# Optimization experiments

Measured on AMD Instinct MI355X. Metric: run time of the kernel, lower is better.

Reference implementation:

```python
import jax, jax.numpy as jnp
import numpy as np

B, Hh, Ww, C = 16, 56, 56, 256
NH, WS, SS = 8, 7, 3
HD = C // NH
N = WS * WS
SCALE = HD ** -0.5
EPS = 1e-5


def _rel_pos_index():
    coords = np.stack(np.meshgrid(np.arange(WS), np.arange(WS), indexing='ij'))  # (2, ws, ws)
    cf = coords.reshape(2, -1)
    rc = (cf[:, :, None] - cf[:, None, :]).transpose(1, 2, 0).astype(np.int64)  # (N, N, 2)
    rc[:, :, 0] += WS - 1
    rc[:, :, 1] += WS - 1
    rc[:, :, 0] *= 2 * WS - 1
    return jnp.asarray(rc.sum(-1))  # (N, N)

REL_IDX = _rel_pos_index()


def _shift_mask():
    # standard Swin SW-MSA mask for cyclic shift
    img = np.zeros((1, Hh, Ww, 1), dtype=np.float32)
    cnt = 0
    for hs in (slice(0, -WS), slice(-WS, -SS), slice(-SS, None)):
        for ws_ in (slice(0, -WS), slice(-WS, -SS), slice(-SS, None)):
            img[:, hs, ws_, :] = cnt
            cnt += 1
    mw = img.reshape(1, Hh // WS, WS, Ww // WS, WS, 1).transpose(0, 1, 3, 2, 4, 5).reshape(-1, N)
    am = mw[:, None, :] - mw[:, :, None]
    return jnp.asarray(np.where(am != 0, -100.0, 0.0).astype(np.float32))  # (nW, N, N)


def _ln(x, g, b):
    mu = x.mean(-1, keepdims=True)
    var = ((x - mu) ** 2).mean(-1, keepdims=True)
    return (x - mu) * jax.lax.rsqrt(var + EPS) * g + b


def setup_inputs() -> dict:
    key = jax.random.key(0)
    ks = jax.random.split(key, 8)
    return {
        'x': jax.random.normal(ks[0], (B, Hh * Ww, C), jnp.float32),
        'mask': _shift_mask(),
        'norm1_g': jnp.ones((C,), jnp.float32),
        'norm1_b': jnp.zeros((C,), jnp.float32),
        'qkv_w': jax.random.normal(ks[1], (3 * C, C), jnp.float32) * 0.02,
        'qkv_b': jnp.zeros((3 * C,), jnp.float32),
        'rel_bias': jax.random.normal(ks[2], ((2 * WS - 1) ** 2, NH), jnp.float32) * 0.02,
        'proj_w': jax.random.normal(ks[3], (C, C), jnp.float32) * 0.02,
        'proj_b': jnp.zeros((C,), jnp.float32),
        'norm2_g': jnp.ones((C,), jnp.float32),
        'norm2_b': jnp.zeros((C,), jnp.float32),
        'fc1_w': jax.random.normal(ks[4], (4 * C, C), jnp.float32) * 0.02,
        'fc1_b': jnp.zeros((4 * C,), jnp.float32),
        'fc2_w': jax.random.normal(ks[5], (C, 4 * C), jnp.float32) * 0.02,
        'fc2_b': jnp.zeros((C,), jnp.float32),
    }


def reference(x, mask, norm1_g, norm1_b, qkv_w, qkv_b, rel_bias, proj_w, proj_b,
              norm2_g, norm2_b, fc1_w, fc1_b, fc2_w, fc2_b):
    shortcut = x
    h = _ln(x, norm1_g, norm1_b).reshape(B, Hh, Ww, C)
    # cyclic shift
    h = jnp.roll(h, (-SS, -SS), axis=(1, 2))
    # window partition -> (B*nW, N, C)
    hw = h.reshape(B, Hh // WS, WS, Ww // WS, WS, C).transpose(0, 1, 3, 2, 4, 5).reshape(-1, N, C)
    # qkv projection
    qkv = (hw @ qkv_w.T + qkv_b).reshape(-1, N, 3, NH, HD).transpose(2, 0, 3, 1, 4)
    q, k, v = qkv[0] * SCALE, qkv[1], qkv[2]  # (Bw, NH, N, HD)
    attn = jnp.einsum('bhnd,bhmd->bhnm', q, k)  # (Bw, NH, N, N)
    rpb = rel_bias[REL_IDX.reshape(-1)].reshape(N, N, NH).transpose(2, 0, 1)
    attn = attn + rpb[None]
    nW = mask.shape[0]
    attn = attn.reshape(B, nW, NH, N, N) + mask[None, :, None]
    attn = jax.nn.softmax(attn.reshape(-1, NH, N, N), axis=-1)
    o = jnp.einsum('bhnm,bhmd->bhnd', attn, v).transpose(0, 2, 1, 3).reshape(-1, N, C)
    o = o @ proj_w.T + proj_b
    # window reverse
    o = o.reshape(B, Hh // WS, Ww // WS, WS, WS, C).transpose(0, 1, 3, 2, 4, 5).reshape(B, Hh, Ww, C)
    o = jnp.roll(o, (SS, SS), axis=(1, 2)).reshape(B, Hh * Ww, C)
    x = shortcut + o
    h2 = _ln(x, norm2_g, norm2_b)
    h2 = jax.nn.gelu(h2 @ fc1_w.T + fc1_b, approximate=False)
    return x + (h2 @ fc2_w.T + fc2_b)
```

## Files before the change

### kernel.cpp

```cpp
#include <hip/hip_runtime.h>
#include <cmath>

#define B_    16
#define HH    56
#define WWI   56
#define C_    256
#define NH_   8
#define WS_   7
#define SS_   3
#define HD_   32
#define NTOK  50176
#define NN    49
#define SCALE_ 0.17677669529663689f
#define EPS_  1e-5f

typedef __bf16  bf16x8  __attribute__((ext_vector_type(8)));
typedef float   f32x4   __attribute__((ext_vector_type(4)));
typedef unsigned short ushort8v __attribute__((ext_vector_type(8)));

__device__ __forceinline__ unsigned short f2bf(float f) {
    unsigned int u = __float_as_uint(f);
    unsigned int r = u + 0x7FFFu + ((u >> 16) & 1u);
    return (unsigned short)(r >> 16);
}
__device__ __forceinline__ float bf2f(unsigned short h) {
    return __uint_as_float(((unsigned int)h) << 16);
}
__device__ __forceinline__ float gelu_t(float x) {
    float t = 0.7978845608028654f * (x + 0.044715f * x * x * x);
    float e = __expf(2.0f * t);
    float th = 1.0f - 2.0f * __builtin_amdgcn_rcpf(e + 1.0f);
    return 0.5f * x * (1.0f + th);
}

__device__ __forceinline__ void gload_lds16(const unsigned short* g, unsigned short* l) {
    __builtin_amdgcn_global_load_lds(
        (const __attribute__((address_space(1))) unsigned int*)g,
        (__attribute__((address_space(3))) unsigned int*)l, 16, 0, 0);
}

__global__ __launch_bounds__(256) void convw_k(
    const float* __restrict__ qkvw, const float* __restrict__ projw,
    const float* __restrict__ fc1w, const float* __restrict__ fc2w,
    unsigned short* __restrict__ dst)
{
    int i = blockIdx.x * 256 + threadIdx.x;
    float v;
    if      (i < 196608) v = qkvw[i];
    else if (i < 262144) v = projw[i - 196608];
    else if (i < 524288) v = fc1w[i - 262144];
    else                 v = fc2w[i - 524288];
    dst[i] = f2bf(v);
}

__global__ __launch_bounds__(256) void cb_k(
    const float* __restrict__ mask, const float* __restrict__ relb,
    unsigned short* __restrict__ cb)
{
    int s = blockIdx.x;
    int wi = s >> 3, head = s & 7;
    for (int p = threadIdx.x; p < 2408; p += 256) {
        float v = 0.0f;
        if (p < 2401) {
            int i = p / NN, j = p - i * NN;
            int di = i / 7 - j / 7 + 6, dj = i % 7 - j % 7 + 6;
            v = relb[(di * 13 + dj) * NH_ + head] + mask[(size_t)wi * 2401 + p];
        }
        cb[(size_t)s * 2408 + p] = f2bf(v);
    }
}

__global__ __launch_bounds__(256) void ln_k(
    const float* __restrict__ x, const float* __restrict__ g,
    const float* __restrict__ bta, unsigned short* __restrict__ dst, int shifted)
{
    int wave = threadIdx.x >> 6, lane = threadIdx.x & 63;
    int tok = blockIdx.x * 4 + wave;
    const float4 v = *(const float4*)(x + (size_t)tok * C_ + lane * 4);
    float s = v.x + v.y + v.z + v.w;
    float q = v.x*v.x + v.y*v.y + v.z*v.z + v.w*v.w;
    for (int o = 32; o > 0; o >>= 1) { s += __shfl_xor(s, o, 64); q += __shfl_xor(q, o, 64); }
    float mu  = s * (1.0f / C_);
    float var = q * (1.0f / C_) - mu * mu;
    float rs  = rsqrtf(var + EPS_);
    float4 gg = *(const float4*)(g   + lane * 4);
    float4 bb = *(const float4*)(bta + lane * 4);
    float y0 = (v.x - mu) * rs * gg.x + bb.x;
    float y1 = (v.y - mu) * rs * gg.y + bb.y;
    float y2 = (v.z - mu) * rs * gg.z + bb.z;
    float y3 = (v.w - mu) * rs * gg.w + bb.w;
    size_t di;
    if (shifted) {
        int b = tok / 3136, p = tok % 3136;
        int ph = p / 56, pw = p % 56;
        int sh = ph - SS_; if (sh < 0) sh += HH;
        int sw = pw - SS_; if (sw < 0) sw += WWI;
        int bw = b * 64 + (sh / WS_) * 8 + (sw / WS_);
        int n  = (sh % WS_) * WS_ + (sw % WS_);
        di = ((size_t)bw * NN + n) * C_ + lane * 4;
    } else {
        di = (size_t)tok * C_ + lane * 4;
    }
    unsigned int lo = (unsigned int)f2bf(y0) | ((unsigned int)f2bf(y1) << 16);
    unsigned int hi = (unsigned int)f2bf(y2) | ((unsigned int)f2bf(y3) << 16);
    uint2 u; u.x = lo; u.y = hi;
    *(uint2*)(dst + di) = u;
}

template<int EPI, int NT>
__global__ __launch_bounds__(256) void gemm_k(
    const unsigned short* __restrict__ A, const unsigned short* __restrict__ Bt,
    int K, const float* __restrict__ bias,
    const float* __restrict__ resid, float* __restrict__ outF,
    unsigned short* __restrict__ outQ, unsigned short* __restrict__ outK,
    unsigned short* __restrict__ outV)
{
    __shared__ __align__(16) unsigned char smem[49152];
    const int tid = threadIdx.x;
    const int lin = blockIdx.x;
    const int xcd = lin & 7, t = lin >> 3;
    const int m0 = (xcd * 49 + t / NT) * 128;
    const int n0 = (t % NT) * 128;
    const int wave = tid >> 6, lane = tid & 63, quad = lane >> 4, l16 = lane & 15;
    const int wm = wave >> 1, wn = wave & 1;
    const int r0 = tid >> 2;
    const int c0 = (((tid & 3) ^ ((tid >> 3) & 3)) * 8);

    const size_t gA0 = (size_t)(m0 + r0) * K + c0;
    const size_t gA1 = (size_t)(m0 + r0 + 64) * K + c0;
    const size_t gB0 = (size_t)(n0 + r0) * K + c0;
    const size_t gB1 = (size_t)(n0 + r0 + 64) * K + c0;
    const int woff = wave * 512;
    const int sw8 = (quad ^ ((l16 >> 1) & 3)) * 8;

    f32x4 acc[4][4] = {};
    const int nk = K >> 5;
    #pragma unroll
    for (int p = 0; p < 2; ++p) {
        unsigned short* sA = (unsigned short*)(smem + p * 16384);
        unsigned short* sB = sA + 4096;
        const int kp = p << 5;
        gload_lds16(A + gA0 + kp, sA + woff);
        gload_lds16(A + gA1 + kp, sA + woff + 2048);
        gload_lds16(Bt + gB0 + kp, sB + woff);
        gload_lds16(Bt + gB1 + kp, sB + woff + 2048);
    }
    int bufc = 0;
    for (int kk = 0; kk < nk; ++kk) {
        if (kk + 2 < nk) {
            int bufn = bufc + 2; if (bufn >= 3) bufn -= 3;
            unsigned short* sA = (unsigned short*)(smem + bufn * 16384);
            unsigned short* sB = sA + 4096;
            const int k2 = (kk + 2) << 5;
            gload_lds16(A + gA0 + k2, sA + woff);
            gload_lds16(A + gA1 + k2, sA + woff + 2048);
            gload_lds16(Bt + gB0 + k2, sB + woff);
            gload_lds16(Bt + gB1 + k2, sB + woff + 2048);
            __asm volatile("s_waitcnt vmcnt(8)\n\ts_barrier" ::: "memory");
        } else if (kk + 1 < nk) {
            __asm volatile("s_waitcnt vmcnt(4)\n\ts_barrier" ::: "memory");
        } else {
            __asm volatile("s_waitcnt vmcnt(0)\n\ts_barrier" ::: "memory");
        }
        const unsigned short* sA = (const unsigned short*)(smem + bufc * 16384);
        const unsigned short* sB = sA + 4096;
        bf16x8 af[4], bfr[4];
        #pragma unroll
        for (int tt = 0; tt < 4; ++tt) {
            af[tt]  = __builtin_bit_cast(bf16x8, *(const ushort8v*)(sA + (wm * 64 + tt * 16 + l16) * 32 + sw8));
            bfr[tt] = __builtin_bit_cast(bf16x8, *(const ushort8v*)(sB + (wn * 64 + tt * 16 + l16) * 32 + sw8));
        }
        #pragma unroll
        for (int mt = 0; mt < 4; ++mt)
            #pragma unroll
            for (int nt = 0; nt < 4; ++nt)
                acc[mt][nt] = __builtin_amdgcn_mfma_f32_16x16x32_bf16(af[mt], bfr[nt], acc[mt][nt], 0, 0, 0);
        __asm volatile("s_barrier" ::: "memory");
        if (++bufc == 3) bufc = 0;
    }

    float b4[4];
    #pragma unroll
    for (int nt = 0; nt < 4; ++nt) b4[nt] = bias[n0 + wn * 64 + nt * 16 + l16];

    if (EPI == 0 || EPI == 2) {
        unsigned short (*swB)[136] = (unsigned short (*)[136])smem;
        const int seg = n0 >> 8;
        const float qs = (EPI == 0 && seg == 0) ? SCALE_ : 1.0f;
        #pragma unroll
        for (int mt = 0; mt < 4; ++mt)
            #pragma unroll
            for (int nt = 0; nt < 4; ++nt)
                #pragma unroll
                for (int r = 0; r < 4; ++r) {
                    float v = acc[mt][nt][r] + b4[nt];
                    if (EPI == 0) v *= qs; else v = gelu_t(v);
                    swB[wm * 64 + mt * 16 + quad * 4 + r][wn * 64 + nt * 16 + l16] = f2bf(v);
                }
        __syncthreads();
        if (EPI == 0) {
            unsigned short* dstp = seg == 0 ? outQ : (seg == 1 ? outK : outV);
            const int nbase = n0 & 255;
            for (int tt = tid; tt < 2048; tt += 256) {
                int row = tt >> 4, c8 = (tt & 15) * 8;
                int m = m0 + row, bw = m / NN, nw = m - bw * NN;
                int cc = nbase + c8;
                uint4 u = *(uint4*)&swB[row][c8];
                *(uint4*)&dstp[(((size_t)bw * NH_ + (cc >> 5)) * NN + nw) * HD_ + (cc & 31)] = u;
            }
        } else {
            for (int tt = tid; tt < 2048; tt += 256) {
                int row = tt >> 4, c8 = (tt & 15) * 8;
                uint4 u = *(uint4*)&swB[row][c8];
                *(uint4*)&outQ[(size_t)(m0 + row) * 1024 + n0 + c8] = u;
            }
        }
    } else {
        float (*swF)[132] = (float (*)[132])smem;
        #pragma unroll
        for (int p = 0; p < 2; ++p) {
            __syncthreads();
            if (wm == p) {
                #pragma unroll
                for (int mt = 0; mt < 4; ++mt)
                    #pragma unroll
                    for (int nt = 0; nt < 4; ++nt)
                        #pragma unroll
                        for (int r = 0; r < 4; ++r)
                            swF[mt * 16 + quad * 4 + r][wn * 64 + nt * 16 + l16] = acc[mt][nt][r] + b4[nt];
            }
            __syncthreads();
            for (int tt = tid; tt < 2048; tt += 256) {
                int rl = tt >> 5, c4 = (tt & 31) * 4;
                size_t adr;
                if (EPI == 1) {
                    int m = m0 + p * 64 + rl, bw = m / NN, nw = m - bw * NN;
                    int b = bw >> 6, wi = bw & 63;
                    int sh = (wi >> 3) * WS_ + nw / WS_;
                    int sw = (wi & 7) * WS_ + nw % WS_;
                    int ph = sh + SS_; if (ph >= HH)  ph -= HH;
                    int pw = sw + SS_; if (pw >= WWI) pw -= WWI;
                    adr = ((size_t)b * 3136 + ph * 56 + pw) * C_ + n0 + c4;
                } else {
                    adr = (size_t)(m0 + p * 64 + rl) * C_ + n0 + c4;
                }
                float4 u = *(float4*)&swF[rl][c4];
                const float4 rr = (EPI == 1) ? *(const float4*)&resid[adr]
                                             : *(const float4*)&outF[adr];
                u.x += rr.x; u.y += rr.y; u.z += rr.z; u.w += rr.w;
                *(float4*)&outF[adr] = u;
            }
        }
    }
}

__global__ __launch_bounds__(256) void attn_k(
    const unsigned short* __restrict__ qb, const unsigned short* __restrict__ kb,
    const unsigned short* __restrict__ vb, const unsigned short* __restrict__ cb,
    unsigned short* __restrict__ ob)
{
    __shared__ unsigned short qs[64][40];
    __shared__ unsigned short ks[64][40];
    __shared__ unsigned short vt[32][72];
    __shared__ unsigned short sp[64][72];
    __shared__ unsigned short cbs[2408];
    const int tid = threadIdx.x;
    const int bw = blockIdx.x >> 3, head = blockIdx.x & 7;
    const size_t base = (size_t)blockIdx.x * (NN * HD_);

    for (int t = tid; t < 588; t += 256) {
        int seg = t / 196, idx = t - seg * 196;
        int e = idx * 8;
        const unsigned short* src = (seg == 0 ? qb : seg == 1 ? kb : vb) + base + e;
        uint4 u = *(const uint4*)src;
        if (seg == 0)      *(uint4*)&qs[e >> 5][e & 31] = u;
        else if (seg == 1) *(uint4*)&ks[e >> 5][e & 31] = u;
        else {
            int n = e >> 5, hd = e & 31;
            const unsigned short* pu = (const unsigned short*)&u;
            #pragma unroll
            for (int uu = 0; uu < 8; ++uu) vt[hd + uu][n] = pu[uu];
        }
    }
    {
        const unsigned short* cbase = cb + (size_t)(((bw & 63) * 8 + head)) * 2408;
        for (int t = tid; t < 301; t += 256)
            *(uint4*)&cbs[t * 8] = *(const uint4*)(cbase + t * 8);
        for (int t = tid; t < 480; t += 256) vt[t / 15][NN + t % 15] = 0;
    }
    __syncthreads();

    const int wave = tid >> 6, lane = tid & 63, quad = lane >> 4, l16 = lane & 15;
    const f32x4 zz = {};

    bf16x8 afq = __builtin_bit_cast(bf16x8, *(const ushort8v*)&qs[wave * 16 + l16][quad * 8]);
    f32x4 s4[4];
    #pragma unroll
    for (int jt = 0; jt < 4; ++jt) {
        bf16x8 bk = __builtin_bit_cast(bf16x8, *(const ushort8v*)&ks[jt * 16 + l16][quad * 8]);
        s4[jt] = __builtin_amdgcn_mfma_f32_16x16x32_bf16(afq, bk, zz, 0, 0, 0);
    }

    #pragma unroll
    for (int r = 0; r < 4; ++r) {
        int i = wave * 16 + quad * 4 + r;
        float vals[4];
        #pragma unroll
        for (int jt = 0; jt < 4; ++jt) {
            int j = jt * 16 + l16;
            vals[jt] = (i < NN && j < NN) ? s4[jt][r] + bf2f(cbs[i * NN + j]) : -1e30f;
        }
        float mx = fmaxf(fmaxf(vals[0], vals[1]), fmaxf(vals[2], vals[3]));
        #pragma unroll
        for (int o = 1; o < 16; o <<= 1) mx = fmaxf(mx, __shfl_xor(mx, o, 64));
        float e[4], sum = 0.0f;
        #pragma unroll
        for (int jt = 0; jt < 4; ++jt) { e[jt] = __expf(vals[jt] - mx); sum += e[jt]; }
        #pragma unroll
        for (int o = 1; o < 16; o <<= 1) sum += __shfl_xor(sum, o, 64);
        float inv = 1.0f / sum;
        #pragma unroll
        for (int jt = 0; jt < 4; ++jt) sp[i][jt * 16 + l16] = f2bf(e[jt] * inv);
    }
    __syncthreads();

    bf16x8 ap[2];
    #pragma unroll
    for (int kt = 0; kt < 2; ++kt)
        ap[kt] = __builtin_bit_cast(bf16x8, *(const ushort8v*)&sp[wave * 16 + l16][kt * 32 + quad * 8]);
    f32x4 o4[2] = {};
    #pragma unroll
    for (int nt = 0; nt < 2; ++nt)
        #pragma unroll
        for (int kt = 0; kt < 2; ++kt) {
            bf16x8 bv = __builtin_bit_cast(bf16x8, *(const ushort8v*)&vt[nt * 16 + l16][kt * 32 + quad * 8]);
            o4[nt] = __builtin_amdgcn_mfma_f32_16x16x32_bf16(ap[kt], bv, o4[nt], 0, 0, 0);
        }
    #pragma unroll
    for (int nt = 0; nt < 2; ++nt)
        #pragma unroll
        for (int r = 0; r < 4; ++r) {
            int i = wave * 16 + quad * 4 + r;
            if (i < NN)
                ob[((size_t)bw * NN + i) * C_ + head * HD_ + nt * 16 + l16] = f2bf(o4[nt][r]);
        }
}

extern "C" void kernel_launch(void* const* d_in, const int* in_sizes, int n_in,
                              void* d_out, int out_size, void* d_ws, size_t ws_size,
                              hipStream_t stream)
{
    const float* x     = (const float*)d_in[0];
    const float* mask  = (const float*)d_in[1];
    const float* n1g   = (const float*)d_in[2];
    const float* n1b   = (const float*)d_in[3];
    const float* qkvw  = (const float*)d_in[4];
    const float* qkvb  = (const float*)d_in[5];
    const float* relb  = (const float*)d_in[6];
    const float* projw = (const float*)d_in[7];
    const float* projb = (const float*)d_in[8];
    const float* n2g   = (const float*)d_in[9];
    const float* n2b   = (const float*)d_in[10];
    const float* fc1w  = (const float*)d_in[11];
    const float* fc1b  = (const float*)d_in[12];
    const float* fc2w  = (const float*)d_in[13];
    const float* fc2b  = (const float*)d_in[14];
    float* out = (float*)d_out;

    unsigned short* wq = (unsigned short*)d_ws;
    unsigned short* wp = wq + 196608;
    unsigned short* w1 = wq + 262144;
    unsigned short* w2 = wq + 524288;
    unsigned short* hw = wq + 786432;
    unsigned short* qb = hw + 12845056;
    unsigned short* kb = qb + 12845056;
    unsigned short* vb = kb + 12845056;
    unsigned short* ob = vb + 12845056;
    unsigned short* h2 = ob + 12845056;
    unsigned short* a1 = h2 + 12845056;
    unsigned short* cbt = a1;

    convw_k<<<3072, 256, 0, stream>>>(qkvw, projw, fc1w, fc2w, wq);
    cb_k<<<512, 256, 0, stream>>>(mask, relb, cbt);
    ln_k<<<12544, 256, 0, stream>>>(x, n1g, n1b, hw, 1);
    gemm_k<0, 6><<<392 * 6, 256, 0, stream>>>(hw, wq, 256, qkvb, nullptr, nullptr, qb, kb, vb);
    attn_k<<<8192, 256, 0, stream>>>(qb, kb, vb, cbt, ob);
    gemm_k<1, 2><<<392 * 2, 256, 0, stream>>>(ob, wp, 256, projb, x, out, nullptr, nullptr, nullptr);
    ln_k<<<12544, 256, 0, stream>>>(out, n2g, n2b, h2, 0);
    gemm_k<2, 8><<<392 * 8, 256, 0, stream>>>(h2, w1, 256, fc1b, nullptr, nullptr, a1, nullptr, nullptr);
    gemm_k<3, 2><<<392 * 2, 256, 0, stream>>>(a1, w2, 1024, fc2b, nullptr, out, nullptr, nullptr, nullptr);
}
```

Measured before the change: 375.2 us.

## Replace direct-to-LDS triple buffering with register-staged double-buffered GEMM pipeline

```diff
diff --git a/kernel.cpp b/kernel.cpp
--- a/kernel.cpp
+++ b/kernel.cpp
@@ -31,12 +31,6 @@
     float e = __expf(2.0f * t);
     float th = 1.0f - 2.0f * __builtin_amdgcn_rcpf(e + 1.0f);
     return 0.5f * x * (1.0f + th);
-}
-
-__device__ __forceinline__ void gload_lds16(const unsigned short* g, unsigned short* l) {
-    __builtin_amdgcn_global_load_lds(
-        (const __attribute__((address_space(1))) unsigned int*)g,
-        (__attribute__((address_space(3))) unsigned int*)l, 16, 0, 0);
 }
 
 __global__ __launch_bounds__(256) void convw_k(
@@ -115,7 +109,7 @@
     unsigned short* __restrict__ outQ, unsigned short* __restrict__ outK,
     unsigned short* __restrict__ outV)
 {
-    __shared__ __align__(16) unsigned char smem[49152];
+    __shared__ __align__(16) unsigned char smem[34816];
     const int tid = threadIdx.x;
     const int lin = blockIdx.x;
     const int xcd = lin & 7, t = lin >> 3;
@@ -126,58 +120,70 @@
     const int r0 = tid >> 2;
     const int c0 = (((tid & 3) ^ ((tid >> 3) & 3)) * 8);
 
-    const size_t gA0 = (size_t)(m0 + r0) * K + c0;
-    const size_t gA1 = (size_t)(m0 + r0 + 64) * K + c0;
-    const size_t gB0 = (size_t)(n0 + r0) * K + c0;
-    const size_t gB1 = (size_t)(n0 + r0 + 64) * K + c0;
-    const int woff = wave * 512;
+    const unsigned short* pA0 = A  + (size_t)(m0 + r0) * K + c0;
+    const unsigned short* pA1 = A  + (size_t)(m0 + r0 + 64) * K + c0;
+    const unsigned short* pB0 = Bt + (size_t)(n0 + r0) * K + c0;
+    const unsigned short* pB1 = Bt + (size_t)(n0 + r0 + 64) * K + c0;
+    unsigned char* stg = smem + tid * 16;
     const int sw8 = (quad ^ ((l16 >> 1) & 3)) * 8;
 
     f32x4 acc[4][4] = {};
     const int nk = K >> 5;
-    #pragma unroll
-    for (int p = 0; p < 2; ++p) {
-        unsigned short* sA = (unsigned short*)(smem + p * 16384);
-        unsigned short* sB = sA + 4096;
-        const int kp = p << 5;
-        gload_lds16(A + gA0 + kp, sA + woff);
-        gload_lds16(A + gA1 + kp, sA + woff + 2048);
-        gload_lds16(Bt + gB0 + kp, sB + woff);
-        gload_lds16(Bt + gB1 + kp, sB + woff + 2048);
-    }
-    int bufc = 0;
-    for (int kk = 0; kk < nk; ++kk) {
+
+    uint4 rA0[2], rA1[2], rB0[2], rB1[2];
+    rA0[0] = *(const uint4*)(pA0);      rA1[0] = *(const uint4*)(pA1);
+    rB0[0] = *(const uint4*)(pB0);      rB1[0] = *(const uint4*)(pB1);
+    rA0[1] = *(const uint4*)(pA0 + 32); rA1[1] = *(const uint4*)(pA1 + 32);
+    rB0[1] = *(const uint4*)(pB0 + 32); rB1[1] = *(const uint4*)(pB1 + 32);
+    *(uint4*)(stg        ) = rA0[0];
+    *(uint4*)(stg +  4096) = rA1[0];
+    *(uint4*)(stg +  8192) = rB0[0];
+    *(uint4*)(stg + 12288) = rB1[0];
+    __asm volatile("s_waitcnt lgkmcnt(0)\n\ts_barrier" ::: "memory");
+
+    #define COMPUTE(p_) { \
+        const unsigned short* sA = (const unsigned short*)(smem + (p_) * 16384); \
+        const unsigned short* sB = sA + 4096; \
+        bf16x8 af[4], bfr[4]; \
+        _Pragma("unroll") \
+        for (int tt = 0; tt < 4; ++tt) { \
+            af[tt]  = __builtin_bit_cast(bf16x8, *(const ushort8v*)(sA + (wm * 64 + tt * 16 + l16) * 32 + sw8)); \
+            bfr[tt] = __builtin_bit_cast(bf16x8, *(const ushort8v*)(sB + (wn * 64 + tt * 16 + l16) * 32 + sw8)); \
+        } \
+        _Pragma("unroll") \
+        for (int mt = 0; mt < 4; ++mt) \
+            _Pragma("unroll") \
+            for (int nt = 0; nt < 4; ++nt) \
+                acc[mt][nt] = __builtin_amdgcn_mfma_f32_16x16x32_bf16(af[mt], bfr[nt], acc[mt][nt], 0, 0, 0); }
+
+    for (int kk = 0; kk < nk; kk += 2) {
         if (kk + 2 < nk) {
-            int bufn = bufc + 2; if (bufn >= 3) bufn -= 3;
-            unsigned short* sA = (unsigned short*)(smem + bufn * 16384);
-            unsigned short* sB = sA + 4096;
             const int k2 = (kk + 2) << 5;
-            gload_lds16(A + gA0 + k2, sA + woff);
-            gload_lds16(A + gA1 + k2, sA + woff + 2048);
-            gload_lds16(Bt + gB0 + k2, sB + woff);
-            gload_lds16(Bt + gB1 + k2, sB + woff + 2048);
-            __asm volatile("s_waitcnt vmcnt(8)\n\ts_barrier" ::: "memory");
-        } else if (kk + 1 < nk) {
-            __asm volatile("s_waitcnt vmcnt(4)\n\ts_barrier" ::: "memory");
-        } else {
-            __asm volatile("s_waitcnt vmcnt(0)\n\ts_barrier" ::: "memory");
-        }
-        const unsigned short* sA = (const unsigned short*)(smem + bufc * 16384);
-        const unsigned short* sB = sA + 4096;
-        bf16x8 af[4], bfr[4];
-        #pragma unroll
-        for (int tt = 0; tt < 4; ++tt) {
-            af[tt]  = __builtin_bit_cast(bf16x8, *(const ushort8v*)(sA + (wm * 64 + tt * 16 + l16) * 32 + sw8));
-            bfr[tt] = __builtin_bit_cast(bf16x8, *(const ushort8v*)(sB + (wn * 64 + tt * 16 + l16) * 32 + sw8));
-        }
-        #pragma unroll
-        for (int mt = 0; mt < 4; ++mt)
-            #pragma unroll
-            for (int nt = 0; nt < 4; ++nt)
-                acc[mt][nt] = __builtin_amdgcn_mfma_f32_16x16x32_bf16(af[mt], bfr[nt], acc[mt][nt], 0, 0, 0);
-        __asm volatile("s_barrier" ::: "memory");
-        if (++bufc == 3) bufc = 0;
-    }
+            rA0[0] = *(const uint4*)(pA0 + k2); rA1[0] = *(const uint4*)(pA1 + k2);
+            rB0[0] = *(const uint4*)(pB0 + k2); rB1[0] = *(const uint4*)(pB1 + k2);
+        }
+        COMPUTE(0);
+        *(uint4*)(stg + 16384        ) = rA0[1];
+        *(uint4*)(stg + 16384 +  4096) = rA1[1];
+        *(uint4*)(stg + 16384 +  8192) = rB0[1];
+        *(uint4*)(stg + 16384 + 12288) = rB1[1];
+        __asm volatile("s_waitcnt lgkmcnt(0)\n\ts_barrier" ::: "memory");
+
+        if (kk + 3 < nk) {
+            const int k3 = (kk + 3) << 5;
+            rA0[1] = *(const uint4*)(pA0 + k3); rA1[1] = *(const uint4*)(pA1 + k3);
+            rB0[1] = *(const uint4*)(pB0 + k3); rB1[1] = *(const uint4*)(pB1 + k3);
+        }
+        COMPUTE(1);
+        if (kk + 2 < nk) {
+            *(uint4*)(stg        ) = rA0[0];
+            *(uint4*)(stg +  4096) = rA1[0];
+            *(uint4*)(stg +  8192) = rB0[0];
+            *(uint4*)(stg + 12288) = rB1[0];
+        }
+        __asm volatile("s_waitcnt lgkmcnt(0)\n\ts_barrier" ::: "memory");
+    }
+    #undef COMPUTE
 
     float b4[4];
     #pragma unroll
```

Measured after the change: 691.9 us. +84.4%, slower.

## Enlarge GEMM tiles to 256x128 and remap workgroups across XCDs

Applied to the files above, without the earlier changes.

```diff
diff --git a/kernel.cpp b/kernel.cpp
--- a/kernel.cpp
+++ b/kernel.cpp
@@ -108,76 +108,75 @@
 }
 
 template<int EPI, int NT>
-__global__ __launch_bounds__(256) void gemm_k(
+__global__ __launch_bounds__(256, 2) void gemm_k(
     const unsigned short* __restrict__ A, const unsigned short* __restrict__ Bt,
     int K, const float* __restrict__ bias,
     const float* __restrict__ resid, float* __restrict__ outF,
     unsigned short* __restrict__ outQ, unsigned short* __restrict__ outK,
     unsigned short* __restrict__ outV)
 {
-    __shared__ __align__(16) unsigned char smem[49152];
+    __shared__ __align__(16) unsigned char smem[73728];
     const int tid = threadIdx.x;
-    const int lin = blockIdx.x;
-    const int xcd = lin & 7, t = lin >> 3;
-    const int m0 = (xcd * 49 + t / NT) * 128;
-    const int n0 = (t % NT) * 128;
+    const int nwg = 196 * NT;
+    const int xcd = blockIdx.x & 7, t = blockIdx.x >> 3;
+    const int wg = xcd * (nwg >> 3) + t;
+    const int m0 = (wg / NT) * 256;
+    const int n0 = (wg % NT) * 128;
     const int wave = tid >> 6, lane = tid & 63, quad = lane >> 4, l16 = lane & 15;
     const int wm = wave >> 1, wn = wave & 1;
-    const int r0 = tid >> 2;
-    const int c0 = (((tid & 3) ^ ((tid >> 3) & 3)) * 8);
-
-    const size_t gA0 = (size_t)(m0 + r0) * K + c0;
-    const size_t gA1 = (size_t)(m0 + r0 + 64) * K + c0;
-    const size_t gB0 = (size_t)(n0 + r0) * K + c0;
-    const size_t gB1 = (size_t)(n0 + r0 + 64) * K + c0;
-    const int woff = wave * 512;
+    const int c0 = (((lane & 3) ^ ((lane >> 3) & 3)) * 8);
+    const unsigned short* p6[6];
+    unsigned dof[6];
+    #pragma unroll
+    for (int i = 0; i < 6; ++i) {
+        int id = wave * 6 + i;
+        p6[i] = (id < 16 ? A  + (size_t)(m0 + id * 16 + (lane >> 2)) * K
+                         : Bt + (size_t)(n0 + (id - 16) * 16 + (lane >> 2)) * K) + c0;
+        dof[i] = id * 1024;
+    }
     const int sw8 = (quad ^ ((l16 >> 1) & 3)) * 8;
 
-    f32x4 acc[4][4] = {};
+    f32x4 acc[8][4] = {};
     const int nk = K >> 5;
-    #pragma unroll
-    for (int p = 0; p < 2; ++p) {
-        unsigned short* sA = (unsigned short*)(smem + p * 16384);
-        unsigned short* sB = sA + 4096;
-        const int kp = p << 5;
-        gload_lds16(A + gA0 + kp, sA + woff);
-        gload_lds16(A + gA1 + kp, sA + woff + 2048);
-        gload_lds16(Bt + gB0 + kp, sB + woff);
-        gload_lds16(Bt + gB1 + kp, sB + woff + 2048);
-    }
+
+    #define STAGE(kt_, p_) { \
+        unsigned char* bb_ = smem + (p_) * 24576; \
+        const int ko_ = (kt_) << 5; \
+        _Pragma("unroll") \
+        for (int i_ = 0; i_ < 6; ++i_) \
+            gload_lds16(p6[i_] + ko_, (unsigned short*)(bb_ + dof[i_])); }
+
+    STAGE(0, 0);
+    STAGE(1, 1);
     int bufc = 0;
     for (int kk = 0; kk < nk; ++kk) {
         if (kk + 2 < nk) {
             int bufn = bufc + 2; if (bufn >= 3) bufn -= 3;
-            unsigned short* sA = (unsigned short*)(smem + bufn * 16384);
-            unsigned short* sB = sA + 4096;
-            const int k2 = (kk + 2) << 5;
-            gload_lds16(A + gA0 + k2, sA + woff);
-            gload_lds16(A + gA1 + k2, sA + woff + 2048);
-            gload_lds16(Bt + gB0 + k2, sB + woff);
-            gload_lds16(Bt + gB1 + k2, sB + woff + 2048);
-            __asm volatile("s_waitcnt vmcnt(8)\n\ts_barrier" ::: "memory");
+            STAGE(kk + 2, bufn);
+            __asm volatile("s_waitcnt vmcnt(12)\n\ts_barrier" ::: "memory");
         } else if (kk + 1 < nk) {
-            __asm volatile("s_waitcnt vmcnt(4)\n\ts_barrier" ::: "memory");
+            __asm volatile("s_waitcnt vmcnt(6)\n\ts_barrier" ::: "memory");
         } else {
             __asm volatile("s_waitcnt vmcnt(0)\n\ts_barrier" ::: "memory");
         }
-        const unsigned short* sA = (const unsigned short*)(smem + bufc * 16384);
-        const unsigned short* sB = sA + 4096;
-        bf16x8 af[4], bfr[4];
-        #pragma unroll
-        for (int tt = 0; tt < 4; ++tt) {
-            af[tt]  = __builtin_bit_cast(bf16x8, *(const ushort8v*)(sA + (wm * 64 + tt * 16 + l16) * 32 + sw8));
+        const unsigned short* sA = (const unsigned short*)(smem + bufc * 24576);
+        const unsigned short* sB = sA + 8192;
+        bf16x8 af[8], bfr[4];
+        #pragma unroll
+        for (int tt = 0; tt < 8; ++tt)
+            af[tt]  = __builtin_bit_cast(bf16x8, *(const ushort8v*)(sA + (wm * 128 + tt * 16 + l16) * 32 + sw8));
+        #pragma unroll
+        for (int tt = 0; tt < 4; ++tt)
             bfr[tt] = __builtin_bit_cast(bf16x8, *(const ushort8v*)(sB + (wn * 64 + tt * 16 + l16) * 32 + sw8));
-        }
-        #pragma unroll
-        for (int mt = 0; mt < 4; ++mt)
+        #pragma unroll
+        for (int mt = 0; mt < 8; ++mt)
             #pragma unroll
             for (int nt = 0; nt < 4; ++nt)
                 acc[mt][nt] = __builtin_amdgcn_mfma_f32_16x16x32_bf16(af[mt], bfr[nt], acc[mt][nt], 0, 0, 0);
         __asm volatile("s_barrier" ::: "memory");
         if (++bufc == 3) bufc = 0;
     }
+    #undef STAGE
 
     float b4[4];
     #pragma unroll
@@ -188,20 +187,20 @@
         const int seg = n0 >> 8;
         const float qs = (EPI == 0 && seg == 0) ? SCALE_ : 1.0f;
         #pragma unroll
-        for (int mt = 0; mt < 4; ++mt)
+        for (int mt = 0; mt < 8; ++mt)
             #pragma unroll
             for (int nt = 0; nt < 4; ++nt)
                 #pragma unroll
                 for (int r = 0; r < 4; ++r) {
                     float v = acc[mt][nt][r] + b4[nt];
                     if (EPI == 0) v *= qs; else v = gelu_t(v);
-                    swB[wm * 64 + mt * 16 + quad * 4 + r][wn * 64 + nt * 16 + l16] = f2bf(v);
+                    swB[wm * 128 + mt * 16 + quad * 4 + r][wn * 64 + nt * 16 + l16] = f2bf(v);
                 }
         __syncthreads();
         if (EPI == 0) {
             unsigned short* dstp = seg == 0 ? outQ : (seg == 1 ? outK : outV);
             const int nbase = n0 & 255;
-            for (int tt = tid; tt < 2048; tt += 256) {
+            for (int tt = tid; tt < 4096; tt += 256) {
                 int row = tt >> 4, c8 = (tt & 15) * 8;
                 int m = m0 + row, bw = m / NN, nw = m - bw * NN;
                 int cc = nbase + c8;
@@ -209,7 +208,7 @@
                 *(uint4*)&dstp[(((size_t)bw * NH_ + (cc >> 5)) * NN + nw) * HD_ + (cc & 31)] = u;
             }
         } else {
-            for (int tt = tid; tt < 2048; tt += 256) {
+            for (int tt = tid; tt < 4096; tt += 256) {
                 int row = tt >> 4, c8 = (tt & 15) * 8;
                 uint4 u = *(uint4*)&swB[row][c8];
                 *(uint4*)&outQ[(size_t)(m0 + row) * 1024 + n0 + c8] = u;
@@ -222,7 +221,7 @@
             __syncthreads();
             if (wm == p) {
                 #pragma unroll
-                for (int mt = 0; mt < 4; ++mt)
+                for (int mt = 0; mt < 8; ++mt)
                     #pragma unroll
                     for (int nt = 0; nt < 4; ++nt)
                         #pragma unroll
@@ -230,11 +229,11 @@
                             swF[mt * 16 + quad * 4 + r][wn * 64 + nt * 16 + l16] = acc[mt][nt][r] + b4[nt];
             }
             __syncthreads();
-            for (int tt = tid; tt < 2048; tt += 256) {
+            for (int tt = tid; tt < 4096; tt += 256) {
                 int rl = tt >> 5, c4 = (tt & 31) * 4;
                 size_t adr;
                 if (EPI == 1) {
-                    int m = m0 + p * 64 + rl, bw = m / NN, nw = m - bw * NN;
+                    int m = m0 + p * 128 + rl, bw = m / NN, nw = m - bw * NN;
                     int b = bw >> 6, wi = bw & 63;
                     int sh = (wi >> 3) * WS_ + nw / WS_;
                     int sw = (wi & 7) * WS_ + nw % WS_;
@@ -242,7 +241,7 @@
                     int pw = sw + SS_; if (pw >= WWI) pw -= WWI;
                     adr = ((size_t)b * 3136 + ph * 56 + pw) * C_ + n0 + c4;
                 } else {
-                    adr = (size_t)(m0 + p * 64 + rl) * C_ + n0 + c4;
+                    adr = (size_t)(m0 + p * 128 + rl) * C_ + n0 + c4;
                 }
                 float4 u = *(float4*)&swF[rl][c4];
                 const float4 rr = (EPI == 1) ? *(const float4*)&resid[adr]
@@ -383,10 +382,10 @@
     convw_k<<<3072, 256, 0, stream>>>(qkvw, projw, fc1w, fc2w, wq);
     cb_k<<<512, 256, 0, stream>>>(mask, relb, cbt);
     ln_k<<<12544, 256, 0, stream>>>(x, n1g, n1b, hw, 1);
-    gemm_k<0, 6><<<392 * 6, 256, 0, stream>>>(hw, wq, 256, qkvb, nullptr, nullptr, qb, kb, vb);
+    gemm_k<0, 6><<<196 * 6, 256, 0, stream>>>(hw, wq, 256, qkvb, nullptr, nullptr, qb, kb, vb);
     attn_k<<<8192, 256, 0, stream>>>(qb, kb, vb, cbt, ob);
-    gemm_k<1, 2><<<392 * 2, 256, 0, stream>>>(ob, wp, 256, projb, x, out, nullptr, nullptr, nullptr);
+    gemm_k<1, 2><<<196 * 2, 256, 0, stream>>>(ob, wp, 256, projb, x, out, nullptr, nullptr, nullptr);
     ln_k<<<12544, 256, 0, stream>>>(out, n2g, n2b, h2, 0);
-    gemm_k<2, 8><<<392 * 8, 256, 0, stream>>>(h2, w1, 256, fc1b, nullptr, nullptr, a1, nullptr, nullptr);
-    gemm_k<3, 2><<<392 * 2, 256, 0, stream>>>(a1, w2, 1024, fc2b, nullptr, out, nullptr, nullptr, nullptr);
-}
+    gemm_k<2, 8><<<196 * 8, 256, 0, stream>>>(h2, w1, 256, fc1b, nullptr, nullptr, a1, nullptr, nullptr);
+    gemm_k<3, 2><<<196 * 2, 256, 0, stream>>>(a1, w2, 1024, fc2b, nullptr, out, nullptr, nullptr, nullptr);
+}
```

Result: slower. 401.4 us (+7.0%).

## Shrink GEMM LDS to double-buffer for higher occupancy and merge prep kernels

Applied to the files above, without the earlier changes.

```diff
diff --git a/kernel.cpp b/kernel.cpp
--- a/kernel.cpp
+++ b/kernel.cpp
@@ -39,34 +39,33 @@
         (__attribute__((address_space(3))) unsigned int*)l, 16, 0, 0);
 }
 
-__global__ __launch_bounds__(256) void convw_k(
+__global__ __launch_bounds__(256) void prep_k(
     const float* __restrict__ qkvw, const float* __restrict__ projw,
     const float* __restrict__ fc1w, const float* __restrict__ fc2w,
-    unsigned short* __restrict__ dst)
-{
-    int i = blockIdx.x * 256 + threadIdx.x;
-    float v;
-    if      (i < 196608) v = qkvw[i];
-    else if (i < 262144) v = projw[i - 196608];
-    else if (i < 524288) v = fc1w[i - 262144];
-    else                 v = fc2w[i - 524288];
-    dst[i] = f2bf(v);
-}
-
-__global__ __launch_bounds__(256) void cb_k(
+    unsigned short* __restrict__ dst,
     const float* __restrict__ mask, const float* __restrict__ relb,
     unsigned short* __restrict__ cb)
 {
-    int s = blockIdx.x;
-    int wi = s >> 3, head = s & 7;
-    for (int p = threadIdx.x; p < 2408; p += 256) {
-        float v = 0.0f;
-        if (p < 2401) {
-            int i = p / NN, j = p - i * NN;
-            int di = i / 7 - j / 7 + 6, dj = i % 7 - j % 7 + 6;
-            v = relb[(di * 13 + dj) * NH_ + head] + mask[(size_t)wi * 2401 + p];
-        }
-        cb[(size_t)s * 2408 + p] = f2bf(v);
+    if (blockIdx.x < 3072) {
+        int i = blockIdx.x * 256 + threadIdx.x;
+        float v;
+        if      (i < 196608) v = qkvw[i];
+        else if (i < 262144) v = projw[i - 196608];
+        else if (i < 524288) v = fc1w[i - 262144];
+        else                 v = fc2w[i - 524288];
+        dst[i] = f2bf(v);
+    } else {
+        int s = blockIdx.x - 3072;
+        int wi = s >> 3, head = s & 7;
+        for (int p = threadIdx.x; p < 2408; p += 256) {
+            float v = 0.0f;
+            if (p < 2401) {
+                int i = p / NN, j = p - i * NN;
+                int di = i / 7 - j / 7 + 6, dj = i % 7 - j % 7 + 6;
+                v = relb[(di * 13 + dj) * NH_ + head] + mask[(size_t)wi * 2401 + p];
+            }
+            cb[(size_t)s * 2408 + p] = f2bf(v);
+        }
     }
 }
 
@@ -108,14 +107,14 @@
 }
 
 template<int EPI, int NT>
-__global__ __launch_bounds__(256) void gemm_k(
+__global__ __launch_bounds__(256, 4) void gemm_k(
     const unsigned short* __restrict__ A, const unsigned short* __restrict__ Bt,
     int K, const float* __restrict__ bias,
     const float* __restrict__ resid, float* __restrict__ outF,
     unsigned short* __restrict__ outQ, unsigned short* __restrict__ outK,
     unsigned short* __restrict__ outV)
 {
-    __shared__ __align__(16) unsigned char smem[49152];
+    __shared__ __align__(16) unsigned char smem[32768];
     const int tid = threadIdx.x;
     const int lin = blockIdx.x;
     const int xcd = lin & 7, t = lin >> 3;
@@ -135,34 +134,26 @@
 
     f32x4 acc[4][4] = {};
     const int nk = K >> 5;
-    #pragma unroll
-    for (int p = 0; p < 2; ++p) {
-        unsigned short* sA = (unsigned short*)(smem + p * 16384);
-        unsigned short* sB = sA + 4096;
-        const int kp = p << 5;
-        gload_lds16(A + gA0 + kp, sA + woff);
-        gload_lds16(A + gA1 + kp, sA + woff + 2048);
-        gload_lds16(Bt + gB0 + kp, sB + woff);
-        gload_lds16(Bt + gB1 + kp, sB + woff + 2048);
-    }
-    int bufc = 0;
+
+    #define STAGE(kt_, p_) { \
+        unsigned short* sA_ = (unsigned short*)(smem + (p_) * 16384); \
+        unsigned short* sB_ = sA_ + 4096; \
+        const int kp_ = (kt_) << 5; \
+        gload_lds16(A + gA0 + kp_, sA_ + woff); \
+        gload_lds16(A + gA1 + kp_, sA_ + woff + 2048); \
+        gload_lds16(Bt + gB0 + kp_, sB_ + woff); \
+        gload_lds16(Bt + gB1 + kp_, sB_ + woff + 2048); }
+
+    STAGE(0, 0);
     for (int kk = 0; kk < nk; ++kk) {
-        if (kk + 2 < nk) {
-            int bufn = bufc + 2; if (bufn >= 3) bufn -= 3;
-            unsigned short* sA = (unsigned short*)(smem + bufn * 16384);
-            unsigned short* sB = sA + 4096;
-            const int k2 = (kk + 2) << 5;
-            gload_lds16(A + gA0 + k2, sA + woff);
-            gload_lds16(A + gA1 + k2, sA + woff + 2048);
-            gload_lds16(Bt + gB0 + k2, sB + woff);
-            gload_lds16(Bt + gB1 + k2, sB + woff + 2048);
-            __asm volatile("s_waitcnt vmcnt(8)\n\ts_barrier" ::: "memory");
-        } else if (kk + 1 < nk) {
+        const int p = kk & 1;
+        if (kk + 1 < nk) {
+            STAGE(kk + 1, p ^ 1);
             __asm volatile("s_waitcnt vmcnt(4)\n\ts_barrier" ::: "memory");
         } else {
             __asm volatile("s_waitcnt vmcnt(0)\n\ts_barrier" ::: "memory");
         }
-        const unsigned short* sA = (const unsigned short*)(smem + bufc * 16384);
+        const unsigned short* sA = (const unsigned short*)(smem + p * 16384);
         const unsigned short* sB = sA + 4096;
         bf16x8 af[4], bfr[4];
         #pragma unroll
@@ -176,8 +167,8 @@
             for (int nt = 0; nt < 4; ++nt)
                 acc[mt][nt] = __builtin_amdgcn_mfma_f32_16x16x32_bf16(af[mt], bfr[nt], acc[mt][nt], 0, 0, 0);
         __asm volatile("s_barrier" ::: "memory");
-        if (++bufc == 3) bufc = 0;
-    }
+    }
+    #undef STAGE
 
     float b4[4];
     #pragma unroll
@@ -187,36 +178,6 @@
         unsigned short (*swB)[136] = (unsigned short (*)[136])smem;
         const int seg = n0 >> 8;
         const float qs = (EPI == 0 && seg == 0) ? SCALE_ : 1.0f;
-        #pragma unroll
-        for (int mt = 0; mt < 4; ++mt)
-            #pragma unroll
-            for (int nt = 0; nt < 4; ++nt)
-                #pragma unroll
-                for (int r = 0; r < 4; ++r) {
-                    float v = acc[mt][nt][r] + b4[nt];
-                    if (EPI == 0) v *= qs; else v = gelu_t(v);
-                    swB[wm * 64 + mt * 16 + quad * 4 + r][wn * 64 + nt * 16 + l16] = f2bf(v);
-                }
-        __syncthreads();
-        if (EPI == 0) {
-            unsigned short* dstp = seg == 0 ? outQ : (seg == 1 ? outK : outV);
-            const int nbase = n0 & 255;
-            for (int tt = tid; tt < 2048; tt += 256) {
-                int row = tt >> 4, c8 = (tt & 15) * 8;
-                int m = m0 + row, bw = m / NN, nw = m - bw * NN;
-                int cc = nbase + c8;
-                uint4 u = *(uint4*)&swB[row][c8];
-                *(uint4*)&dstp[(((size_t)bw * NH_ + (cc >> 5)) * NN + nw) * HD_ + (cc & 31)] = u;
-            }
-        } else {
-            for (int tt = tid; tt < 2048; tt += 256) {
-                int row = tt >> 4, c8 = (tt & 15) * 8;
-                uint4 u = *(uint4*)&swB[row][c8];
-                *(uint4*)&outQ[(size_t)(m0 + row) * 1024 + n0 + c8] = u;
-            }
-        }
-    } else {
-        float (*swF)[132] = (float (*)[132])smem;
         #pragma unroll
         for (int p = 0; p < 2; ++p) {
             __syncthreads();
@@ -226,15 +187,53 @@
                     #pragma unroll
                     for (int nt = 0; nt < 4; ++nt)
                         #pragma unroll
+                        for (int r = 0; r < 4; ++r) {
+                            float v = acc[mt][nt][r] + b4[nt];
+                            if (EPI == 0) v *= qs; else v = gelu_t(v);
+                            swB[mt * 16 + quad * 4 + r][wn * 64 + nt * 16 + l16] = f2bf(v);
+                        }
+            }
+            __syncthreads();
+            if (EPI == 0) {
+                unsigned short* dstp = seg == 0 ? outQ : (seg == 1 ? outK : outV);
+                const int nbase = n0 & 255;
+                for (int tt = tid; tt < 1024; tt += 256) {
+                    int row = tt >> 4, c8 = (tt & 15) * 8;
+                    int m = m0 + p * 64 + row, bw = m / NN, nw = m - bw * NN;
+                    int cc = nbase + c8;
+                    uint4 u = *(uint4*)&swB[row][c8];
+                    *(uint4*)&dstp[(((size_t)bw * NH_ + (cc >> 5)) * NN + nw) * HD_ + (cc & 31)] = u;
+                }
+            } else {
+                for (int tt = tid; tt < 1024; tt += 256) {
+                    int row = tt >> 4, c8 = (tt & 15) * 8;
+                    uint4 u = *(uint4*)&swB[row][c8];
+                    *(uint4*)&outQ[(size_t)(m0 + p * 64 + row) * 1024 + n0 + c8] = u;
+                }
+            }
+        }
+    } else {
+        float (*swF)[132] = (float (*)[132])smem;
+        #pragma unroll
+        for (int p = 0; p < 4; ++p) {
+            __syncthreads();
+            if (wm == (p >> 1)) {
+                const int mtb = (p & 1) * 2;
+                #pragma unroll
+                for (int mt = 0; mt < 2; ++mt)
+                    #pragma unroll
+                    for (int nt = 0; nt < 4; ++nt)
+                        #pragma unroll
                         for (int r = 0; r < 4; ++r)
-                            swF[mt * 16 + quad * 4 + r][wn * 64 + nt * 16 + l16] = acc[mt][nt][r] + b4[nt];
+                            swF[mt * 16 + quad * 4 + r][wn * 64 + nt * 16 + l16] =
+                                acc[mtb + mt][nt][r] + b4[nt];
             }
             __syncthreads();
-            for (int tt = tid; tt < 2048; tt += 256) {
+            for (int tt = tid; tt < 1024; tt += 256) {
                 int rl = tt >> 5, c4 = (tt & 31) * 4;
                 size_t adr;
                 if (EPI == 1) {
-                    int m = m0 + p * 64 + rl, bw = m / NN, nw = m - bw * NN;
+                    int m = m0 + p * 32 + rl, bw = m / NN, nw = m - bw * NN;
                     int b = bw >> 6, wi = bw & 63;
                     int sh = (wi >> 3) * WS_ + nw / WS_;
                     int sw = (wi & 7) * WS_ + nw % WS_;
@@ -242,7 +241,7 @@
                     int pw = sw + SS_; if (pw >= WWI) pw -= WWI;
                     adr = ((size_t)b * 3136 + ph * 56 + pw) * C_ + n0 + c4;
                 } else {
-                    adr = (size_t)(m0 + p * 64 + rl) * C_ + n0 + c4;
+                    adr = (size_t)(m0 + p * 32 + rl) * C_ + n0 + c4;
                 }
                 float4 u = *(float4*)&swF[rl][c4];
                 const float4 rr = (EPI == 1) ? *(const float4*)&resid[adr]
@@ -380,8 +379,7 @@
     unsigned short* a1 = h2 + 12845056;
     unsigned short* cbt = a1;
 
-    convw_k<<<3072, 256, 0, stream>>>(qkvw, projw, fc1w, fc2w, wq);
-    cb_k<<<512, 256, 0, stream>>>(mask, relb, cbt);
+    prep_k<<<3584, 256, 0, stream>>>(qkvw, projw, fc1w, fc2w, wq, mask, relb, cbt);
     ln_k<<<12544, 256, 0, stream>>>(x, n1g, n1b, hw, 1);
     gemm_k<0, 6><<<392 * 6, 256, 0, stream>>>(hw, wq, 256, qkvb, nullptr, nullptr, qb, kb, vb);
     attn_k<<<8192, 256, 0, stream>>>(qb, kb, vb, cbt, ob);
```

Measured after the change: 372.9 us. About the same (-0.6%).
